# Kernel optimization log

Measured on AMD Instinct MI355X. Metric: run time of the kernel, lower is better.

Reference implementation:

```python
import jax, jax.numpy as jnp
import numpy as np

NUM_ROUTING = 3

def squash(s):
    # squash along the unit_size axis (axis=2), exactly as the torch module
    mag_sq = jnp.sum(s * s, axis=2, keepdims=True)
    mag = jnp.sqrt(mag_sq)
    return mag_sq / (1.0 + mag_sq) * (s / mag)

def setup_inputs() -> dict:
    key = jax.random.key(0)
    k1, k2 = jax.random.split(key)
    B, in_unit, in_channel = 512, 8, 1152
    num_unit, unit_size = 10, 16
    x = jax.random.normal(k1, (B, in_unit, in_channel), dtype=jnp.float32)
    weight = jax.random.normal(k2, (in_channel, num_unit, unit_size, in_unit), dtype=jnp.float32)
    return {"x": x, "weight": weight}

def reference(x, weight):
    B = x.shape[0]
    C, J = weight.shape[0], weight.shape[1]  # in_channel, num_unit
    xt = jnp.swapaxes(x, 1, 2)  # [B, C, in_unit]
    # u_hat[c, j, b, s] = W[c, j, s, :] @ x[b, c, :]
    u_hat = jnp.einsum('cjsi,bci->cjbs', weight, xt)  # [C, J, B, S]
    b_ij = jnp.zeros((C, J), dtype=x.dtype)
    v = None
    for _ in range(NUM_ROUTING):
        # DGL degree-bucketing puts all J capsule nodes in one bucket, so the
        # softmax(dim=0) in capsule_reduce is over the num_unit axis per input capsule
        c = jax.nn.softmax(b_ij, axis=1)          # [C, J]
        s = jnp.einsum('cj,cjbs->jbs', c, u_hat)  # [J, B, S]
        v = squash(s)                             # [J, B, S]
        # update_edge: b_ij += mean over batch of <v_j, u_hat_ij>
        b_ij = b_ij + jnp.einsum('jbs,cjbs->cj', v, u_hat) / B
    # [J, B, S] -> [B, J, S] -> unsqueeze(1).unsqueeze(4).squeeze(1) -> [B, J, S, 1]
    return jnp.transpose(v, (1, 0, 2))[..., None]
```

## Files before the change

### kernel.cpp

```cpp
#include <hip/hip_runtime.h>
#include <hip/hip_bf16.h>
#include <math.h>

#define B_  512
#define I_  8
#define C_  1152
#define J_  10
#define S_  16
#define K1  9216
#define NKB 288
#define KBT 16

typedef short short8 __attribute__((ext_vector_type(8)));
typedef float floatx4 __attribute__((ext_vector_type(4)));

__device__ inline unsigned short f2bf(float f) {
    unsigned int u = __float_as_uint(f);
    return (unsigned short)((u + 0x7FFFu + ((u >> 16) & 1u)) >> 16);
}
__device__ inline unsigned int pack2(float a, float b) {
    __hip_bfloat162 h = __float22bfloat162_rn(float2{a, b});
    return *reinterpret_cast<unsigned int*>(&h);
}

__global__ __launch_bounds__(512) void k_pack(const float* __restrict__ x,
                                              const float* __restrict__ W,
                                              uint4* __restrict__ Bs,
                                              uint4* __restrict__ Bt,
                                              uint4* __restrict__ Wf,
                                              unsigned short* __restrict__ W2,
                                              float* __restrict__ b_ij) {
    __shared__ float lds[10240];
    const int task = blockIdx.x;
    const int t = threadIdx.x;
    const int w = t >> 6, L = t & 63, quad = L >> 4;

    if (task < 576) {
        const int bt = task / 36, kt = task % 36;
        const int b0 = bt * 32, k0 = kt * 256;
        #pragma unroll
        for (int p = 0; p < 4; p++) {
            int f4 = p * 512 + t;
            int row = f4 >> 6, c4 = (f4 & 63) << 2;
            *(float4*)&lds[row * 260 + c4] =
                *(const float4*)&x[(size_t)(b0 + row) * K1 + k0 + c4];
        }
        __syncthreads();
        #pragma unroll
        for (int p = 0; p < 2; p++) {
            const int bl = p * 16 + (L & 15);
            const float* s = &lds[bl * 260 + w * 32 + quad * 8];
            uint4 o;
            o.x = pack2(s[0], s[1]); o.y = pack2(s[2], s[3]);
            o.z = pack2(s[4], s[5]); o.w = pack2(s[6], s[7]);
            Bs[((size_t)(bt * 2 + p) * NKB + kt * 8 + w) * 64 + L] = o;
        }
        #pragma unroll
        for (int p = 0; p < 2; p++) {
            const int ntl = w * 2 + p;
            const int nl = ntl * 16 + (L & 15);
            float v[8];
            #pragma unroll
            for (int e = 0; e < 8; e++) v[e] = lds[(quad * 8 + e) * 260 + nl];
            uint4 o;
            o.x = pack2(v[0], v[1]); o.y = pack2(v[2], v[3]);
            o.z = pack2(v[4], v[5]); o.w = pack2(v[6], v[7]);
            Bt[((size_t)(kt * 16 + ntl) * KBT + bt) * 64 + L] = o;
        }
    } else if (task < 720) {
        const int c0 = (task - 576) * 8;
        #pragma unroll
        for (int p = 0; p < 5; p++) {
            int f4 = p * 512 + t;
            int cc = f4 / 320, off4 = (f4 % 320) << 2;
            *(float4*)&lds[cc * 1280 + off4] =
                *(const float4*)&W[(size_t)(c0 + cc) * 1280 + off4];
        }
        __syncthreads();
        #pragma unroll
        for (int p = 0; p < 3; p++) {
            int o = p * 512 + t;
            if (o < 1280) {
                int j = o >> 7, i = (o >> 4) & 7, m = o & 15;
                int k0w = i * C_ + c0;
                int Lw = m | (((k0w >> 3) & 3) << 4);
                float v[8];
                #pragma unroll
                for (int e = 0; e < 8; e++)
                    v[e] = lds[e * 1280 + j * 128 + m * 8 + i];
                uint4 og;
                og.x = pack2(v[0], v[1]); og.y = pack2(v[2], v[3]);
                og.z = pack2(v[4], v[5]); og.w = pack2(v[6], v[7]);
                Wf[((size_t)j * NKB + (k0w >> 5)) * 64 + Lw] = og;
            }
        }
        #pragma unroll
        for (int p = 0; p < 2; p++) {
            int o = p * 512 + t;
            if (o < 640) {
                int j = o >> 6, i = (o >> 3) & 7, cc = o & 7;
                unsigned int r8[8];
                #pragma unroll
                for (int h = 0; h < 8; h++)
                    r8[h] = pack2(lds[cc * 1280 + j * 128 + (2 * h) * 8 + i],
                                  lds[cc * 1280 + j * 128 + (2 * h + 1) * 8 + i]);
                unsigned short* dst = W2 + ((size_t)(j * 8 + i) * C_ + c0 + cc) * 16;
                *(uint4*)dst       = make_uint4(r8[0], r8[1], r8[2], r8[3]);
                *(uint4*)(dst + 8) = make_uint4(r8[4], r8[5], r8[6], r8[7]);
            }
        }
    } else {
        for (int idx = t; idx < C_ * J_; idx += 512) b_ij[idx] = 0.0f;
    }
}

__global__ __launch_bounds__(512) void k_sgemm_f(const short8* __restrict__ Wf,
                                                 const short8* __restrict__ Bs,
                                                 const float* __restrict__ b_ij,
                                                 unsigned short* __restrict__ Vf,
                                                 float* __restrict__ out,
                                                 int mode) {
    __shared__ float smf[1152 + 2048];
    const int t = threadIdx.x, w = t >> 6, L = t & 63, quad = L >> 4;
    const int bid = blockIdx.x;
    const int xcd = bid & 7, sl = bid >> 3;
    const int j  = 5 * (xcd >> 2) + sl % 5;
    const int nt = 8 * (xcd & 3) + sl / 5;

    if (mode) {
        for (int c = t; c < C_; c += 512) {
            float bv[J_], mx = -1e30f;
            #pragma unroll
            for (int jj = 0; jj < J_; jj++) {
                bv[jj] = b_ij[c * J_ + jj]; mx = fmaxf(mx, bv[jj]);
            }
            float sum = 0.0f;
            #pragma unroll
            for (int jj = 0; jj < J_; jj++) sum += __expf(bv[jj] - mx);
            smf[c] = __expf(bv[j] - mx) / sum;
        }
    }
    __syncthreads();

    const short8* pA = Wf + ((size_t)j * NKB + w * 36) * 64 + L;
    const short8* pB = Bs + ((size_t)nt * NKB + w * 36) * 64 + L;
    floatx4 acc = {0.f, 0.f, 0.f, 0.f};
    if (mode) {
        #pragma unroll 6
        for (int i = 0; i < 36; i++) {
            short8 a = pA[i * 64];
            const int cb = i * 32 + quad * 8;
            float4 cl = *(const float4*)&smf[cb];
            float4 ch = *(const float4*)&smf[cb + 4];
            float cn8[8] = {cl.x, cl.y, cl.z, cl.w, ch.x, ch.y, ch.z, ch.w};
            unsigned int* au = (unsigned int*)&a;
            short8 a2; unsigned int* ao = (unsigned int*)&a2;
            #pragma unroll
            for (int h = 0; h < 4; h++) {
                float f0 = __uint_as_float(au[h] << 16)         * cn8[2 * h];
                float f1 = __uint_as_float(au[h] & 0xffff0000u) * cn8[2 * h + 1];
                ao[h] = pack2(f0, f1);
            }
            acc = __builtin_amdgcn_mfma_f32_16x16x32_bf16(a2, pB[i * 64], acc, 0, 0, 0);
        }
    } else {
        #pragma unroll 6
        for (int i = 0; i < 36; i++)
            acc = __builtin_amdgcn_mfma_f32_16x16x32_bf16(pA[i * 64], pB[i * 64], acc, 0, 0, 0);
    }

    const int col = L & 15, rw = quad << 2;
    float* base = &smf[1152 + w * 256];
    #pragma unroll
    for (int r = 0; r < 4; r++)
        base[(rw + r) * 16 + col] = acc[r];
    __syncthreads();

    if (t < 16) {
        float sv[S_]; float msq = 0.f;
        #pragma unroll
        for (int s = 0; s < S_; s++) {
            float a = 0.f;
            #pragma unroll
            for (int w8 = 0; w8 < 8; w8++)
                a += smf[1152 + w8 * 256 + s * 16 + t];
            if (mode == 0) a *= 0.1f;
            sv[s] = a; msq += a * a;
        }
        const float scale = msq / ((1.f + msq) * sqrtf(msq));
        const int b = nt * 16 + t;
        if (mode < 2) {
            const int kb = b >> 5, lh = (b >> 3) & 3, e = b & 7;
            #pragma unroll
            for (int s = 0; s < S_; s++)
                Vf[((size_t)(j * KBT + kb) * 64 + (s | (lh << 4))) * 8 + e] =
                    f2bf(sv[s] * scale);
        } else {
            float o16[S_];
            #pragma unroll
            for (int s = 0; s < S_; s++) o16[s] = sv[s] * scale;
            float* dst = &out[((size_t)b * J_ + j) * S_];
            #pragma unroll
            for (int r4 = 0; r4 < 4; r4++)
                *(float4*)(dst + r4 * 4) = *(float4*)(o16 + r4 * 4);
        }
    }
}

__global__ __launch_bounds__(512) void k_tgemm_bup(const short8* __restrict__ Vf,
                                                   const short8* __restrict__ Bt,
                                                   const unsigned short* __restrict__ W2,
                                                   float* __restrict__ b_ij) {
    __shared__ float red[8][16];
    const int t = threadIdx.x, w = t >> 6, L = t & 63;
    const int bid = blockIdx.x;
    const int xcd = bid & 7, sl = bid >> 3;
    const int cblk = 9 * xcd + sl / 10;
    const int j    = sl % 10;
    const int nt   = w * 72 + cblk;
    const short8* pA = Vf + (size_t)j * KBT * 64 + L;
    const short8* pB = Bt + (size_t)nt * KBT * 64 + L;
    floatx4 a = {0.f, 0.f, 0.f, 0.f};
    #pragma unroll
    for (int kb = 0; kb < KBT; kb++)
        a = __builtin_amdgcn_mfma_f32_16x16x32_bf16(pA[kb * 64], pB[kb * 64], a, 0, 0, 0);
    const int col = L & 15, rw = (L >> 4) << 2;
    const int c = cblk * 16 + col;
    const unsigned short* wp = W2 + ((size_t)(j * 8 + w) * C_ + c) * 16 + rw;
    uint2 wv = *(const uint2*)wp;
    float p = a[0] * __uint_as_float((unsigned int)wv.x << 16)
            + a[1] * __uint_as_float(wv.x & 0xffff0000u)
            + a[2] * __uint_as_float((unsigned int)wv.y << 16)
            + a[3] * __uint_as_float(wv.y & 0xffff0000u);
    p += __shfl_xor(p, 16);
    p += __shfl_xor(p, 32);
    if ((L >> 4) == 0) red[w][col] = p;
    __syncthreads();
    if (t < 16) {
        float acc = 0.f;
        #pragma unroll
        for (int w8 = 0; w8 < 8; w8++) acc += red[w8][t];
        const size_t idx = (size_t)(cblk * 16 + t) * J_ + j;
        b_ij[idx] += acc * (1.0f / 512.f);
    }
}

extern "C" void kernel_launch(void* const* d_in, const int* in_sizes, int n_in,
                              void* d_out, int out_size, void* d_ws, size_t ws_size,
                              hipStream_t stream) {
    const float* x = (const float*)d_in[0];
    const float* W = (const float*)d_in[1];
    float* out = (float*)d_out;
    float* ws  = (float*)d_ws;

    float* Bs_f = ws;
    float* Bt_f = Bs_f + 2359296;
    float* Wf_f = Bt_f + 2359296;
    float* W2_f = Wf_f + 737280;
    float* Vf_f = W2_f + 737280;
    float* bij  = Vf_f + 40960;

    k_pack<<<721, 512, 0, stream>>>(x, W, (uint4*)Bs_f, (uint4*)Bt_f,
                                    (uint4*)Wf_f, (unsigned short*)W2_f, bij);

    k_sgemm_f<<<320, 512, 0, stream>>>(
        (const short8*)Wf_f, (const short8*)Bs_f, bij,
        (unsigned short*)Vf_f, out, 0);
    k_tgemm_bup<<<720, 512, 0, stream>>>(
        (const short8*)Vf_f, (const short8*)Bt_f, (const unsigned short*)W2_f, bij);

    k_sgemm_f<<<320, 512, 0, stream>>>(
        (const short8*)Wf_f, (const short8*)Bs_f, bij,
        (unsigned short*)Vf_f, out, 1);
    k_tgemm_bup<<<720, 512, 0, stream>>>(
        (const short8*)Vf_f, (const short8*)Bt_f, (const unsigned short*)W2_f, bij);

    k_sgemm_f<<<320, 512, 0, stream>>>(
        (const short8*)Wf_f, (const short8*)Bs_f, bij,
        (unsigned short*)Vf_f, out, 2);
}
```

Before: 129.9 us.

## Fuse routing stages into three kernels using grid-wide atomic barriers

Merges the pack, s-GEMM, and t-GEMM/b_ij-update stages so each of three launches runs one stage, crosses a global atomic-counter barrier, then 320 of its blocks run the following s-GEMM. This removes three kernel launches and their inter-launch gaps. It also parallelises the squash epilogue across 256 threads using shuffle reductions instead of 16 serial threads. The barrier relies on all 721/720 blocks being co-resident (launch bounds of 8 blocks per CU), and it adds a memset before the first launch.

New measurement: 346.1 us. 167% more time.

```diff
diff --git a/kernel.cpp b/kernel.cpp
--- a/kernel.cpp
+++ b/kernel.cpp
@@ -23,14 +23,115 @@
     return *reinterpret_cast<unsigned int*>(&h);
 }
 
-__global__ __launch_bounds__(512) void k_pack(const float* __restrict__ x,
-                                              const float* __restrict__ W,
-                                              uint4* __restrict__ Bs,
-                                              uint4* __restrict__ Bt,
-                                              uint4* __restrict__ Wf,
-                                              unsigned short* __restrict__ W2,
-                                              float* __restrict__ b_ij) {
+__device__ __forceinline__ void barrier_arrive_wait(int* bar, int target, bool wait) {
+    __syncthreads();
+    if (threadIdx.x == 0) {
+        __hip_atomic_fetch_add(bar, 1, __ATOMIC_RELEASE, __HIP_MEMORY_SCOPE_AGENT);
+        if (wait) {
+            while (__hip_atomic_load(bar, __ATOMIC_RELAXED, __HIP_MEMORY_SCOPE_AGENT) < target)
+                __builtin_amdgcn_s_sleep(8);
+            __threadfence();
+        }
+    }
+    __syncthreads();
+}
+
+template<int MODE>
+__device__ __forceinline__ void sgemm_body(float* smf,
+        const short8* __restrict__ Wf, const short8* __restrict__ Bs,
+        const float* __restrict__ b_ij, unsigned short* __restrict__ Vf,
+        float* __restrict__ out, int bid) {
+    const int t = threadIdx.x, w = t >> 6, L = t & 63, quad = L >> 4;
+    const int xcd = bid & 7, sl = bid >> 3;
+    const int j  = 5 * (xcd >> 2) + sl % 5;
+    const int nt = 8 * (xcd & 3) + sl / 5;
+
+    if (MODE) {
+        for (int c = t; c < C_; c += 512) {
+            float bv[J_], mx = -1e30f;
+            #pragma unroll
+            for (int jj = 0; jj < J_; jj++) {
+                bv[jj] = b_ij[c * J_ + jj]; mx = fmaxf(mx, bv[jj]);
+            }
+            float sum = 0.0f;
+            #pragma unroll
+            for (int jj = 0; jj < J_; jj++) sum += __expf(bv[jj] - mx);
+            smf[c] = __expf(bv[j] - mx) / sum;
+        }
+    }
+    __syncthreads();
+
+    const short8* pA = Wf + ((size_t)j * NKB + w * 36) * 64 + L;
+    const short8* pB = Bs + ((size_t)nt * NKB + w * 36) * 64 + L;
+    floatx4 acc = {0.f, 0.f, 0.f, 0.f};
+    if (MODE) {
+        #pragma unroll 6
+        for (int i = 0; i < 36; i++) {
+            short8 a = pA[i * 64];
+            const int cb = i * 32 + quad * 8;
+            float4 cl = *(const float4*)&smf[cb];
+            float4 ch = *(const float4*)&smf[cb + 4];
+            float cn8[8] = {cl.x, cl.y, cl.z, cl.w, ch.x, ch.y, ch.z, ch.w};
+            unsigned int* au = (unsigned int*)&a;
+            short8 a2; unsigned int* ao = (unsigned int*)&a2;
+            #pragma unroll
+            for (int h = 0; h < 4; h++) {
+                float f0 = __uint_as_float(au[h] << 16)         * cn8[2 * h];
+                float f1 = __uint_as_float(au[h] & 0xffff0000u) * cn8[2 * h + 1];
+                ao[h] = pack2(f0, f1);
+            }
+            acc = __builtin_amdgcn_mfma_f32_16x16x32_bf16(a2, pB[i * 64], acc, 0, 0, 0);
+        }
+    } else {
+        #pragma unroll 6
+        for (int i = 0; i < 36; i++)
+            acc = __builtin_amdgcn_mfma_f32_16x16x32_bf16(pA[i * 64], pB[i * 64], acc, 0, 0, 0);
+    }
+
+    const int col = L & 15, rw = quad << 2;
+    float* base = &smf[1152 + w * 256];
+    #pragma unroll
+    for (int r = 0; r < 4; r++)
+        base[(rw + r) * 16 + col] = acc[r];
+    __syncthreads();
+
+    if (t < 256) {
+        const int bl = t >> 4, s = t & 15;
+        float a = 0.f;
+        #pragma unroll
+        for (int w8 = 0; w8 < 8; w8++)
+            a += smf[1152 + w8 * 256 + s * 16 + bl];
+        if (MODE == 0) a *= 0.1f;
+        float msq = a * a;
+        #pragma unroll
+        for (int m = 1; m < 16; m <<= 1) msq += __shfl_xor(msq, m);
+        const float scale = msq / ((1.f + msq) * sqrtf(msq));
+        const float sv = a * scale;
+        const int b = nt * 16 + bl;
+        if (MODE < 2) {
+            const int kb = b >> 5, lh = (b >> 3) & 3, e = b & 7;
+            Vf[((size_t)(j * KBT + kb) * 64 + (s | (lh << 4))) * 8 + e] = f2bf(sv);
+        } else {
+            out[((size_t)b * J_ + j) * S_ + s] = sv;
+        }
+    }
+}
+
+__global__ __launch_bounds__(512, 8) void k_pack_s0(const float* __restrict__ x,
+        const float* __restrict__ W, float* __restrict__ ws,
+        float* __restrict__ out, int* __restrict__ bar) {
     __shared__ float lds[10240];
+    float* Bs_f = ws;
+    float* Bt_f = Bs_f + 2359296;
+    float* Wf_f = Bt_f + 2359296;
+    float* W2_f = Wf_f + 737280;
+    float* Vf_f = W2_f + 737280;
+    float* bij  = Vf_f + 40960;
+    uint4* Bs = (uint4*)Bs_f;
+    uint4* Bt = (uint4*)Bt_f;
+    uint4* Wf = (uint4*)Wf_f;
+    unsigned short* W2 = (unsigned short*)W2_f;
+
     const int task = blockIdx.x;
     const int t = threadIdx.x;
     const int w = t >> 6, L = t & 63, quad = L >> 4;
@@ -110,139 +211,72 @@
             }
         }
     } else {
-        for (int idx = t; idx < C_ * J_; idx += 512) b_ij[idx] = 0.0f;
-    }
-}
-
-__global__ __launch_bounds__(512) void k_sgemm_f(const short8* __restrict__ Wf,
-                                                 const short8* __restrict__ Bs,
-                                                 const float* __restrict__ b_ij,
-                                                 unsigned short* __restrict__ Vf,
-                                                 float* __restrict__ out,
-                                                 int mode) {
-    __shared__ float smf[1152 + 2048];
-    const int t = threadIdx.x, w = t >> 6, L = t & 63, quad = L >> 4;
-    const int bid = blockIdx.x;
-    const int xcd = bid & 7, sl = bid >> 3;
-    const int j  = 5 * (xcd >> 2) + sl % 5;
-    const int nt = 8 * (xcd & 3) + sl / 5;
-
-    if (mode) {
-        for (int c = t; c < C_; c += 512) {
-            float bv[J_], mx = -1e30f;
-            #pragma unroll
-            for (int jj = 0; jj < J_; jj++) {
-                bv[jj] = b_ij[c * J_ + jj]; mx = fmaxf(mx, bv[jj]);
-            }
-            float sum = 0.0f;
-            #pragma unroll
-            for (int jj = 0; jj < J_; jj++) sum += __expf(bv[jj] - mx);
-            smf[c] = __expf(bv[j] - mx) / sum;
-        }
-    }
-    __syncthreads();
-
-    const short8* pA = Wf + ((size_t)j * NKB + w * 36) * 64 + L;
-    const short8* pB = Bs + ((size_t)nt * NKB + w * 36) * 64 + L;
-    floatx4 acc = {0.f, 0.f, 0.f, 0.f};
-    if (mode) {
-        #pragma unroll 6
-        for (int i = 0; i < 36; i++) {
-            short8 a = pA[i * 64];
-            const int cb = i * 32 + quad * 8;
-            float4 cl = *(const float4*)&smf[cb];
-            float4 ch = *(const float4*)&smf[cb + 4];
-            float cn8[8] = {cl.x, cl.y, cl.z, cl.w, ch.x, ch.y, ch.z, ch.w};
-            unsigned int* au = (unsigned int*)&a;
-            short8 a2; unsigned int* ao = (unsigned int*)&a2;
-            #pragma unroll
-            for (int h = 0; h < 4; h++) {
-                float f0 = __uint_as_float(au[h] << 16)         * cn8[2 * h];
-                float f1 = __uint_as_float(au[h] & 0xffff0000u) * cn8[2 * h + 1];
-                ao[h] = pack2(f0, f1);
-            }
-            acc = __builtin_amdgcn_mfma_f32_16x16x32_bf16(a2, pB[i * 64], acc, 0, 0, 0);
-        }
-    } else {
-        #pragma unroll 6
-        for (int i = 0; i < 36; i++)
-            acc = __builtin_amdgcn_mfma_f32_16x16x32_bf16(pA[i * 64], pB[i * 64], acc, 0, 0, 0);
-    }
-
-    const int col = L & 15, rw = quad << 2;
-    float* base = &smf[1152 + w * 256];
-    #pragma unroll
-    for (int r = 0; r < 4; r++)
-        base[(rw + r) * 16 + col] = acc[r];
-    __syncthreads();
-
-    if (t < 16) {
-        float sv[S_]; float msq = 0.f;
-        #pragma unroll
-        for (int s = 0; s < S_; s++) {
-            float a = 0.f;
-            #pragma unroll
-            for (int w8 = 0; w8 < 8; w8++)
-                a += smf[1152 + w8 * 256 + s * 16 + t];
-            if (mode == 0) a *= 0.1f;
-            sv[s] = a; msq += a * a;
-        }
-        const float scale = msq / ((1.f + msq) * sqrtf(msq));
-        const int b = nt * 16 + t;
-        if (mode < 2) {
-            const int kb = b >> 5, lh = (b >> 3) & 3, e = b & 7;
-            #pragma unroll
-            for (int s = 0; s < S_; s++)
-                Vf[((size_t)(j * KBT + kb) * 64 + (s | (lh << 4))) * 8 + e] =
-                    f2bf(sv[s] * scale);
-        } else {
-            float o16[S_];
-            #pragma unroll
-            for (int s = 0; s < S_; s++) o16[s] = sv[s] * scale;
-            float* dst = &out[((size_t)b * J_ + j) * S_];
-            #pragma unroll
-            for (int r4 = 0; r4 < 4; r4++)
-                *(float4*)(dst + r4 * 4) = *(float4*)(o16 + r4 * 4);
-        }
-    }
-}
-
-__global__ __launch_bounds__(512) void k_tgemm_bup(const short8* __restrict__ Vf,
-                                                   const short8* __restrict__ Bt,
-                                                   const unsigned short* __restrict__ W2,
-                                                   float* __restrict__ b_ij) {
-    __shared__ float red[8][16];
+        for (int idx = t; idx < C_ * J_; idx += 512) bij[idx] = 0.0f;
+    }
+
+    const bool part = blockIdx.x < 320;
+    barrier_arrive_wait(bar, 721, part);
+    if (!part) return;
+
+    sgemm_body<0>(lds, (const short8*)Wf_f, (const short8*)Bs_f, bij,
+                  (unsigned short*)Vf_f, out, blockIdx.x);
+}
+
+template<int MODE>
+__global__ __launch_bounds__(512, 8) void k_t_s(float* __restrict__ ws,
+        float* __restrict__ out, int* __restrict__ bar) {
+    __shared__ float lds[3200];
+    float* Bs_f = ws;
+    float* Bt_f = Bs_f + 2359296;
+    float* Wf_f = Bt_f + 2359296;
+    float* W2_f = Wf_f + 737280;
+    float* Vf_f = W2_f + 737280;
+    float* bij  = Vf_f + 40960;
+    const short8* Vf = (const short8*)Vf_f;
+    const short8* Bt = (const short8*)Bt_f;
+    const unsigned short* W2 = (const unsigned short*)W2_f;
+
+    float (*red)[16] = (float(*)[16])lds;
     const int t = threadIdx.x, w = t >> 6, L = t & 63;
     const int bid = blockIdx.x;
-    const int xcd = bid & 7, sl = bid >> 3;
-    const int cblk = 9 * xcd + sl / 10;
-    const int j    = sl % 10;
-    const int nt   = w * 72 + cblk;
-    const short8* pA = Vf + (size_t)j * KBT * 64 + L;
-    const short8* pB = Bt + (size_t)nt * KBT * 64 + L;
-    floatx4 a = {0.f, 0.f, 0.f, 0.f};
-    #pragma unroll
-    for (int kb = 0; kb < KBT; kb++)
-        a = __builtin_amdgcn_mfma_f32_16x16x32_bf16(pA[kb * 64], pB[kb * 64], a, 0, 0, 0);
-    const int col = L & 15, rw = (L >> 4) << 2;
-    const int c = cblk * 16 + col;
-    const unsigned short* wp = W2 + ((size_t)(j * 8 + w) * C_ + c) * 16 + rw;
-    uint2 wv = *(const uint2*)wp;
-    float p = a[0] * __uint_as_float((unsigned int)wv.x << 16)
-            + a[1] * __uint_as_float(wv.x & 0xffff0000u)
-            + a[2] * __uint_as_float((unsigned int)wv.y << 16)
-            + a[3] * __uint_as_float(wv.y & 0xffff0000u);
-    p += __shfl_xor(p, 16);
-    p += __shfl_xor(p, 32);
-    if ((L >> 4) == 0) red[w][col] = p;
-    __syncthreads();
-    if (t < 16) {
-        float acc = 0.f;
-        #pragma unroll
-        for (int w8 = 0; w8 < 8; w8++) acc += red[w8][t];
-        const size_t idx = (size_t)(cblk * 16 + t) * J_ + j;
-        b_ij[idx] += acc * (1.0f / 512.f);
-    }
+    {
+        const int xcd = bid & 7, sl = bid >> 3;
+        const int cblk = 9 * xcd + sl / 10;
+        const int j    = sl % 10;
+        const int nt   = w * 72 + cblk;
+        const short8* pA = Vf + (size_t)j * KBT * 64 + L;
+        const short8* pB = Bt + (size_t)nt * KBT * 64 + L;
+        floatx4 a = {0.f, 0.f, 0.f, 0.f};
+        #pragma unroll
+        for (int kb = 0; kb < KBT; kb++)
+            a = __builtin_amdgcn_mfma_f32_16x16x32_bf16(pA[kb * 64], pB[kb * 64], a, 0, 0, 0);
+        const int col = L & 15, rw = (L >> 4) << 2;
+        const int c = cblk * 16 + col;
+        const unsigned short* wp = W2 + ((size_t)(j * 8 + w) * C_ + c) * 16 + rw;
+        uint2 wv = *(const uint2*)wp;
+        float p = a[0] * __uint_as_float((unsigned int)wv.x << 16)
+                + a[1] * __uint_as_float(wv.x & 0xffff0000u)
+                + a[2] * __uint_as_float((unsigned int)wv.y << 16)
+                + a[3] * __uint_as_float(wv.y & 0xffff0000u);
+        p += __shfl_xor(p, 16);
+        p += __shfl_xor(p, 32);
+        if ((L >> 4) == 0) red[w][col] = p;
+        __syncthreads();
+        if (t < 16) {
+            float acc = 0.f;
+            #pragma unroll
+            for (int w8 = 0; w8 < 8; w8++) acc += red[w8][t];
+            const size_t idx = (size_t)(cblk * 16 + t) * J_ + j;
+            bij[idx] += acc * (1.0f / 512.f);
+        }
+    }
+
+    const bool part = bid < 320;
+    barrier_arrive_wait(bar, 720, part);
+    if (!part) return;
+
+    sgemm_body<MODE>(lds, (const short8*)Wf_f, (const short8*)Bs_f, bij,
+                     (unsigned short*)Vf_f, out, bid);
 }
 
 extern "C" void kernel_launch(void* const* d_in, const int* in_sizes, int n_in,
@@ -253,29 +287,10 @@
     float* out = (float*)d_out;
     float* ws  = (float*)d_ws;
 
-    float* Bs_f = ws;
-    float* Bt_f = Bs_f + 2359296;
-    float* Wf_f = Bt_f + 2359296;
-    float* W2_f = Wf_f + 737280;
-    float* Vf_f = W2_f + 737280;
-    float* bij  = Vf_f + 40960;
-
-    k_pack<<<721, 512, 0, stream>>>(x, W, (uint4*)Bs_f, (uint4*)Bt_f,
-                                    (uint4*)Wf_f, (unsigned short*)W2_f, bij);
-
-    k_sgemm_f<<<320, 512, 0, stream>>>(
-        (const short8*)Wf_f, (const short8*)Bs_f, bij,
-        (unsigned short*)Vf_f, out, 0);
-    k_tgemm_bup<<<720, 512, 0, stream>>>(
-        (const short8*)Vf_f, (const short8*)Bt_f, (const unsigned short*)W2_f, bij);
-
-    k_sgemm_f<<<320, 512, 0, stream>>>(
-        (const short8*)Wf_f, (const short8*)Bs_f, bij,
-        (unsigned short*)Vf_f, out, 1);
-    k_tgemm_bup<<<720, 512, 0, stream>>>(
-        (const short8*)Vf_f, (const short8*)Bt_f, (const unsigned short*)W2_f, bij);
-
-    k_sgemm_f<<<320, 512, 0, stream>>>(
-        (const short8*)Wf_f, (const short8*)Bs_f, bij,
-        (unsigned short*)Vf_f, out, 2);
-}
+    int* bar = (int*)(ws + 2359296 * 2 + 737280 * 2 + 40960 + 11520);
+    hipMemsetAsync(bar, 0, 256, stream);
+
+    k_pack_s0<<<721, 512, 0, stream>>>(x, W, ws, out, bar);
+    k_t_s<1><<<720, 512, 0, stream>>>(ws, out, bar + 1);
+    k_t_s<2><<<720, 512, 0, stream>>>(ws, out, bar + 2);
+}
```

## Batch global loads before MFMA chains and parallelize squash epilogue across 256 threads

Applied to the files above, without the earlier changes.

Both GEMM kernels now issue groups of 8-9 global loads into register arrays before running their MFMA chains, so memory latency overlaps instead of serializing per iteration. The W2 load in the b_ij update kernel is hoisted ahead of the MFMA loop. The squash epilogue now uses 256 threads, one per (batch, s) element, with a shuffle reduction for the norm instead of 16 threads looping serially. Launch bounds add a minimum of 4 blocks per CU, which caps register use and may cause spills given the larger register arrays.

Result: no change. 131.1 us (+1.0%).

```diff
diff --git a/kernel.cpp b/kernel.cpp
--- a/kernel.cpp
+++ b/kernel.cpp
@@ -114,12 +114,12 @@
     }
 }
 
-__global__ __launch_bounds__(512) void k_sgemm_f(const short8* __restrict__ Wf,
-                                                 const short8* __restrict__ Bs,
-                                                 const float* __restrict__ b_ij,
-                                                 unsigned short* __restrict__ Vf,
-                                                 float* __restrict__ out,
-                                                 int mode) {
+__global__ __launch_bounds__(512, 4) void k_sgemm_f(const short8* __restrict__ Wf,
+                                                    const short8* __restrict__ Bs,
+                                                    const float* __restrict__ b_ij,
+                                                    unsigned short* __restrict__ Vf,
+                                                    float* __restrict__ out,
+                                                    int mode) {
     __shared__ float smf[1152 + 2048];
     const int t = threadIdx.x, w = t >> 6, L = t & 63, quad = L >> 4;
     const int bid = blockIdx.x;
@@ -146,27 +146,45 @@
     const short8* pB = Bs + ((size_t)nt * NKB + w * 36) * 64 + L;
     floatx4 acc = {0.f, 0.f, 0.f, 0.f};
     if (mode) {
-        #pragma unroll 6
-        for (int i = 0; i < 36; i++) {
-            short8 a = pA[i * 64];
-            const int cb = i * 32 + quad * 8;
-            float4 cl = *(const float4*)&smf[cb];
-            float4 ch = *(const float4*)&smf[cb + 4];
-            float cn8[8] = {cl.x, cl.y, cl.z, cl.w, ch.x, ch.y, ch.z, ch.w};
-            unsigned int* au = (unsigned int*)&a;
-            short8 a2; unsigned int* ao = (unsigned int*)&a2;
-            #pragma unroll
-            for (int h = 0; h < 4; h++) {
-                float f0 = __uint_as_float(au[h] << 16)         * cn8[2 * h];
-                float f1 = __uint_as_float(au[h] & 0xffff0000u) * cn8[2 * h + 1];
-                ao[h] = pack2(f0, f1);
-            }
-            acc = __builtin_amdgcn_mfma_f32_16x16x32_bf16(a2, pB[i * 64], acc, 0, 0, 0);
+        #pragma unroll
+        for (int bb = 0; bb < 4; bb++) {
+            short8 av[9], bv9[9];
+            #pragma unroll
+            for (int u = 0; u < 9; u++) {
+                av[u]  = pA[(bb * 9 + u) * 64];
+                bv9[u] = pB[(bb * 9 + u) * 64];
+            }
+            #pragma unroll
+            for (int u = 0; u < 9; u++) {
+                const int i = bb * 9 + u;
+                const int cb = i * 32 + quad * 8;
+                float4 cl = *(const float4*)&smf[cb];
+                float4 ch = *(const float4*)&smf[cb + 4];
+                float cn8[8] = {cl.x, cl.y, cl.z, cl.w, ch.x, ch.y, ch.z, ch.w};
+                unsigned int* au = (unsigned int*)&av[u];
+                short8 a2; unsigned int* ao = (unsigned int*)&a2;
+                #pragma unroll
+                for (int h = 0; h < 4; h++) {
+                    float f0 = __uint_as_float(au[h] << 16)         * cn8[2 * h];
+                    float f1 = __uint_as_float(au[h] & 0xffff0000u) * cn8[2 * h + 1];
+                    ao[h] = pack2(f0, f1);
+                }
+                acc = __builtin_amdgcn_mfma_f32_16x16x32_bf16(a2, bv9[u], acc, 0, 0, 0);
+            }
         }
     } else {
-        #pragma unroll 6
-        for (int i = 0; i < 36; i++)
-            acc = __builtin_amdgcn_mfma_f32_16x16x32_bf16(pA[i * 64], pB[i * 64], acc, 0, 0, 0);
+        #pragma unroll
+        for (int bb = 0; bb < 4; bb++) {
+            short8 av[9], bv9[9];
+            #pragma unroll
+            for (int u = 0; u < 9; u++) {
+                av[u]  = pA[(bb * 9 + u) * 64];
+                bv9[u] = pB[(bb * 9 + u) * 64];
+            }
+            #pragma unroll
+            for (int u = 0; u < 9; u++)
+                acc = __builtin_amdgcn_mfma_f32_16x16x32_bf16(av[u], bv9[u], acc, 0, 0, 0);
+        }
     }
 
     const int col = L & 15, rw = quad << 2;
@@ -176,41 +194,32 @@
         base[(rw + r) * 16 + col] = acc[r];
     __syncthreads();
 
-    if (t < 16) {
-        float sv[S_]; float msq = 0.f;
-        #pragma unroll
-        for (int s = 0; s < S_; s++) {
-            float a = 0.f;
-            #pragma unroll
-            for (int w8 = 0; w8 < 8; w8++)
-                a += smf[1152 + w8 * 256 + s * 16 + t];
-            if (mode == 0) a *= 0.1f;
-            sv[s] = a; msq += a * a;
-        }
+    if (t < 256) {
+        const int bl = t >> 4, s = t & 15;
+        float a = 0.f;
+        #pragma unroll
+        for (int w8 = 0; w8 < 8; w8++)
+            a += smf[1152 + w8 * 256 + s * 16 + bl];
+        if (mode == 0) a *= 0.1f;
+        float msq = a * a;
+        #pragma unroll
+        for (int m = 1; m < 16; m <<= 1) msq += __shfl_xor(msq, m);
         const float scale = msq / ((1.f + msq) * sqrtf(msq));
-        const int b = nt * 16 + t;
+        const float sv = a * scale;
+        const int b = nt * 16 + bl;
         if (mode < 2) {
             const int kb = b >> 5, lh = (b >> 3) & 3, e = b & 7;
-            #pragma unroll
-            for (int s = 0; s < S_; s++)
-                Vf[((size_t)(j * KBT + kb) * 64 + (s | (lh << 4))) * 8 + e] =
-                    f2bf(sv[s] * scale);
+            Vf[((size_t)(j * KBT + kb) * 64 + (s | (lh << 4))) * 8 + e] = f2bf(sv);
         } else {
-            float o16[S_];
-            #pragma unroll
-            for (int s = 0; s < S_; s++) o16[s] = sv[s] * scale;
-            float* dst = &out[((size_t)b * J_ + j) * S_];
-            #pragma unroll
-            for (int r4 = 0; r4 < 4; r4++)
-                *(float4*)(dst + r4 * 4) = *(float4*)(o16 + r4 * 4);
-        }
-    }
-}
-
-__global__ __launch_bounds__(512) void k_tgemm_bup(const short8* __restrict__ Vf,
-                                                   const short8* __restrict__ Bt,
-                                                   const unsigned short* __restrict__ W2,
-                                                   float* __restrict__ b_ij) {
+            out[((size_t)b * J_ + j) * S_ + s] = sv;
+        }
+    }
+}
+
+__global__ __launch_bounds__(512, 4) void k_tgemm_bup(const short8* __restrict__ Vf,
+                                                      const short8* __restrict__ Bt,
+                                                      const unsigned short* __restrict__ W2,
+                                                      float* __restrict__ b_ij) {
     __shared__ float red[8][16];
     const int t = threadIdx.x, w = t >> 6, L = t & 63;
     const int bid = blockIdx.x;
@@ -220,14 +229,26 @@
     const int nt   = w * 72 + cblk;
     const short8* pA = Vf + (size_t)j * KBT * 64 + L;
     const short8* pB = Bt + (size_t)nt * KBT * 64 + L;
-    floatx4 a = {0.f, 0.f, 0.f, 0.f};
-    #pragma unroll
-    for (int kb = 0; kb < KBT; kb++)
-        a = __builtin_amdgcn_mfma_f32_16x16x32_bf16(pA[kb * 64], pB[kb * 64], a, 0, 0, 0);
+
     const int col = L & 15, rw = (L >> 4) << 2;
     const int c = cblk * 16 + col;
     const unsigned short* wp = W2 + ((size_t)(j * 8 + w) * C_ + c) * 16 + rw;
     uint2 wv = *(const uint2*)wp;
+
+    floatx4 a = {0.f, 0.f, 0.f, 0.f};
+    #pragma unroll
+    for (int bb = 0; bb < 2; bb++) {
+        short8 av[8], bv[8];
+        #pragma unroll
+        for (int u = 0; u < 8; u++) {
+            av[u] = pA[(bb * 8 + u) * 64];
+            bv[u] = pB[(bb * 8 + u) * 64];
+        }
+        #pragma unroll
+        for (int u = 0; u < 8; u++)
+            a = __builtin_amdgcn_mfma_f32_16x16x32_bf16(av[u], bv[u], a, 0, 0, 0);
+    }
+
     float p = a[0] * __uint_as_float((unsigned int)wv.x << 16)
             + a[1] * __uint_as_float(wv.x & 0xffff0000u)
             + a[2] * __uint_as_float((unsigned int)wv.y << 16)
```
